# Kernel optimization log

Measured on AMD Instinct MI355X. Metric: run time of the kernel, lower is better.

The kernel has to match this reference:

```python
import jax, jax.numpy as jnp
import numpy as np
from jax import lax

L, B, T_IMG, T_TXT = 12, 2, 256, 64
E, H, G = 1024, 16, 2730
V = 16416  # image_vocab_count + 1
C = E // H
EPS = 1e-6  # flax LayerNorm default


def _ln(x, scale, bias):
    mu = jnp.mean(x, -1, keepdims=True)
    var = jnp.var(x, -1, keepdims=True)
    y = (x - mu) * lax.rsqrt(var + EPS)
    if scale is not None:
        y = y * scale
    if bias is not None:
        y = y + bias
    return y


def _attend(k, v, q, mask, o_w):
    # k,v: [B,K,H,C]  q: [B,Q,H,C]  mask: [B,K]
    bias = jnp.where(mask, 0.0, -jnp.inf)[:, None, None, :]
    w = jnp.einsum('bqhc,bkhc->bhqk', q, k) + bias
    w = jax.nn.softmax(w, axis=-1)
    out = jnp.einsum('bhqk,bkhc->bqhc', w, v)
    return out.reshape(out.shape[0], out.shape[1], E) @ o_w


def setup_inputs():
    key = jax.random.key(0)
    ks = jax.random.split(key, 16)
    s = 0.02
    n = lambda k, shape: jax.random.normal(k, shape, jnp.float32) * s
    return dict(
        encoder_state=n(ks[0], (B, T_TXT, E)),
        keys_state=jnp.zeros((L, B, T_IMG, H, C), jnp.float32),
        values_state=jnp.zeros((L, B, T_IMG, H, C), jnp.float32),
        attention_mask=jnp.ones((B, T_TXT), jnp.bool_),
        prev_token=5000,
        token_index=100,
        embed_tok=n(ks[1], (V, E)),
        embed_pos=n(ks[2], (T_IMG, E)),
        ln_emb_s=jnp.ones((E,), jnp.float32),
        ln_emb_b=jnp.zeros((E,), jnp.float32),
        final_ln_b=jnp.zeros((E,), jnp.float32),
        lm_head_w=n(ks[3], (E, V)),
        pre_sa_ln_b=jnp.zeros((L, E), jnp.float32),
        sa_q_w=n(ks[4], (L, E, E)), sa_k_w=n(ks[5], (L, E, E)),
        sa_v_w=n(ks[6], (L, E, E)), sa_o_w=n(ks[7], (L, E, E)),
        sa_ln_s=jnp.ones((L, E), jnp.float32), sa_ln_b=jnp.zeros((L, E), jnp.float32),
        pre_ca_ln_b=jnp.zeros((L, E), jnp.float32),
        ca_q_w=n(ks[8], (L, E, E)), ca_k_w=n(ks[9], (L, E, E)),
        ca_v_w=n(ks[10], (L, E, E)), ca_o_w=n(ks[11], (L, E, E)),
        ca_ln_s=jnp.ones((L, E), jnp.float32), ca_ln_b=jnp.zeros((L, E), jnp.float32),
        glu_ln0_b=jnp.zeros((L, E), jnp.float32),
        glu_fc0_w=n(ks[12], (L, E, G)), glu_fc1_w=n(ks[13], (L, E, G)),
        glu_ln1_b=jnp.zeros((L, G), jnp.float32),
        glu_fc2_w=n(ks[14], (L, G, E)),
    )


def _decode_step(encoder_state, keys_state, values_state, attention_mask,
                 prev_token, token_index, embed_tok, embed_pos,
                 ln_emb_s, ln_emb_b, final_ln_b, lm_head_w, layer_params):
    ones = jnp.ones((B, 1), jnp.int32)
    ds = embed_tok[prev_token * ones] + embed_pos[token_index * ones]  # [B,1,E]
    ds = _ln(ds, ln_emb_s, ln_emb_b)
    self_mask = jnp.broadcast_to(jnp.arange(T_IMG) < token_index + 1, (B, T_IMG))
    scale = C ** 0.5

    def step(ds, xs):
        ks_l, vs_l, p = xs  # per-layer KV cache [B,T_IMG,H,C] and params
        (pre_sa_b, qw, kw, vw, ow, sa_s, sa_b,
         pre_ca_b, cqw, ckw, cvw, cow, ca_s, ca_b,
         g0b, f0, f1, g1b, f2) = p
        # --- self attention with KV-cache append ---
        residual = ds
        x = _ln(ds, None, pre_sa_b)
        ks_l = lax.dynamic_update_slice(ks_l, (x @ kw).reshape(B, 1, H, C), (0, token_index, 0, 0))
        vs_l = lax.dynamic_update_slice(vs_l, (x @ vw).reshape(B, 1, H, C), (0, token_index, 0, 0))
        q = (x @ qw).reshape(B, 1, H, C) / scale
        x = _attend(ks_l, vs_l, q, self_mask, ow)
        ds = residual + _ln(x, sa_s, sa_b)
        # --- cross attention over encoder state ---
        residual = ds
        x = _ln(ds, None, pre_ca_b)
        ek = (encoder_state @ ckw).reshape(B, T_TXT, H, C)
        ev = (encoder_state @ cvw).reshape(B, T_TXT, H, C)
        q = (x @ cqw).reshape(B, 1, H, C) / scale
        x = _attend(ek, ev, q, attention_mask, cow)
        ds = residual + _ln(x, ca_s, ca_b)
        # --- GLU FFN ---
        residual = ds
        z = _ln(ds, None, g0b)
        w = jax.nn.gelu(z @ f0, approximate=False)
        z = _ln(w * (z @ f1), None, g1b)
        ds = residual + z @ f2
        return ds, (ks_l, vs_l)

    ds, (keys_state, values_state) = lax.scan(step, ds, (keys_state, values_state, layer_params))
    ds = _ln(ds, None, final_ln_b)
    logits = ds @ lm_head_w  # [B,1,V]
    return logits, keys_state, values_state


def reference(encoder_state, keys_state, values_state, attention_mask, prev_token,
              token_index, embed_tok, embed_pos, ln_emb_s, ln_emb_b, final_ln_b,
              lm_head_w, pre_sa_ln_b, sa_q_w, sa_k_w, sa_v_w, sa_o_w, sa_ln_s,
              sa_ln_b, pre_ca_ln_b, ca_q_w, ca_k_w, ca_v_w, ca_o_w, ca_ln_s,
              ca_ln_b, glu_ln0_b, glu_fc0_w, glu_fc1_w, glu_ln1_b, glu_fc2_w):
    layer_params = (pre_sa_ln_b, sa_q_w, sa_k_w, sa_v_w, sa_o_w, sa_ln_s, sa_ln_b,
                    pre_ca_ln_b, ca_q_w, ca_k_w, ca_v_w, ca_o_w, ca_ln_s, ca_ln_b,
                    glu_ln0_b, glu_fc0_w, glu_fc1_w, glu_ln1_b, glu_fc2_w)
    return _decode_step(encoder_state, keys_state, values_state, attention_mask,
                        prev_token, token_index, embed_tok, embed_pos,
                        ln_emb_s, ln_emb_b, final_ln_b, lm_head_w, layer_params)
```

## Files before the change

### kernel.cpp

```cpp
#include <hip/hip_runtime.h>
#include <math.h>

#define LAYERS 12
#define EE 1024
#define GG 2730
#define VV 16416
#define EPS 1e-6f

#define OFF_DS 0
#define NSLOT 37
#define OFF_ACC (OFF_DS + NSLOT*2048)
#define ACC_STRIDE 28672
#define AQ 0
#define AK 2048
#define AV 4096
#define AY 6144
#define ASC 10240
#define AOUT 12288
#define AY2 14336
#define AA 16384
#define AB2 21844
#define ACC_TOTAL (LAYERS*ACC_STRIDE)
#define ZERO_FLOATS (NSLOT*2048 + ACC_TOTAL)

#define KVL 524288
#define KVB 262144

struct MegaP {
  const float* enc; const float* keys_in; const float* values_in;
  const int* maski; const int* pt; const int* ti;
  const float* tok; const float* pos; const float* ln_s; const float* ln_b;
  const float* final_b; const float* lm_w;
  const float* pre_sa_b; const float* saq; const float* sak; const float* sav;
  const float* sao; const float* sas; const float* sab;
  const float* pre_ca_b; const float* caq; const float* ckw; const float* cvw;
  const float* cao; const float* cas; const float* cab;
  const float* g0b; const float* f0; const float* f1; const float* g1b; const float* f2;
  float* logits; float* keys_out; float* values_out; float* ws;
};

__device__ __forceinline__ void red4(float* sm, float& a, float& b, float& c, float& d){
  #pragma unroll
  for(int o=32;o;o>>=1){ a+=__shfl_down(a,o); b+=__shfl_down(b,o); c+=__shfl_down(c,o); d+=__shfl_down(d,o); }
  int w=threadIdx.x>>6, l=threadIdx.x&63;
  __syncthreads();
  if(l==0){ sm[w]=a; sm[4+w]=b; sm[8+w]=c; sm[12+w]=d; }
  __syncthreads();
  a=sm[0]+sm[1]+sm[2]+sm[3]; b=sm[4]+sm[5]+sm[6]+sm[7];
  c=sm[8]+sm[9]+sm[10]+sm[11]; d=sm[12]+sm[13]+sm[14]+sm[15];
}

__device__ __forceinline__ void ln_stats_g(const float* v, int K, float* sm,
    float& mu0, float& rs0, float& mu1, float& rs1){
  float s0=0,q0=0,s1=0,q1=0;
  for(int i=threadIdx.x;i<K;i+=256){ float a=v[i], b=v[K+i]; s0+=a;q0+=a*a;s1+=b;q1+=b*b; }
  red4(sm,s0,q0,s1,q1);
  mu0=s0/K; mu1=s1/K;
  rs0=rsqrtf(fmaxf(q0/K-mu0*mu0,0.f)+EPS);
  rs1=rsqrtf(fmaxf(q1/K-mu1*mu1,0.f)+EPS);
}

__device__ __forceinline__ void ln_stats_l(float (*Ds)[1024], float* sm,
    float& mu0, float& rs0, float& mu1, float& rs1){
  float s0=0,q0=0,s1=0,q1=0;
  for(int i=threadIdx.x;i<EE;i+=256){ float a=Ds[0][i], b=Ds[1][i]; s0+=a;q0+=a*a;s1+=b;q1+=b*b; }
  red4(sm,s0,q0,s1,q1);
  mu0=s0/EE; mu1=s1/EE;
  rs0=rsqrtf(fmaxf(q0/EE-mu0*mu0,0.f)+EPS);
  rs1=rsqrtf(fmaxf(q1/EE-mu1*mu1,0.f)+EPS);
}

__device__ __forceinline__ void build_ds3(const float* dsi, const float* accL,
    const float* sasl, const float* sabl, const float* casl, const float* cabl,
    float (*Ds)[1024], float* sm){
  float mu0,rs0,mu1,rs1;
  ln_stats_g(accL+AY, EE, sm, mu0,rs0,mu1,rs1);
  for(int i=threadIdx.x;i<EE;i+=256){ float sc=sasl[i], bi=sabl[i];
    Ds[0][i]=dsi[i]    + (accL[AY+i]-mu0)*rs0*sc + bi;
    Ds[1][i]=dsi[EE+i] + (accL[AY+EE+i]-mu1)*rs1*sc + bi; }
  ln_stats_g(accL+AY2, EE, sm, mu0,rs0,mu1,rs1);
  for(int i=threadIdx.x;i<EE;i+=256){ float sc=casl[i], bi=cabl[i];
    Ds[0][i] += (accL[AY2+i]-mu0)*rs0*sc + bi;
    Ds[1][i] += (accL[AY2+EE+i]-mu1)*rs1*sc + bi; }
}

__global__ __launch_bounds__(256)
void k_prelude(MegaP p){
  __shared__ float ev[EE];
  __shared__ float sm[16];
  const int t=threadIdx.x;
  int ptv = p.pt[0], tiv = p.ti[0];
  float s0=0,q0=0,d1=0,d2=0;
  for(int i=t;i<EE;i+=256){ float v=p.tok[(size_t)ptv*EE+i]+p.pos[(size_t)tiv*EE+i]; ev[i]=v; s0+=v; q0+=v*v; }
  red4(sm,s0,q0,d1,d2);
  float mu=s0/EE, rs=rsqrtf(fmaxf(q0/EE-mu*mu,0.f)+EPS);
  float* ds0 = p.ws + OFF_DS;
  __syncthreads();
  for(int i=t;i<EE;i+=256){ float y=(ev[i]-mu)*rs*p.ln_s[i]+p.ln_b[i]; ds0[i]=y; ds0[EE+i]=y; }
}

__global__ __launch_bounds__(256)
void k_qkv(MegaP p, int l){
  __shared__ float Xs[2][1024];
  __shared__ float sm[16];
  const int t=threadIdx.x, bx=blockIdx.x, by=blockIdx.y;
  if (bx >= 12){
    int cb = (bx-12)*64 + by;
    #pragma unroll
    for(int j=0;j<4;j++){
      int idx4 = cb*1024 + j*256 + t;
      int kv = idx4 >> 17;
      int r4 = idx4 & 131071;
      size_t off = (size_t)l*KVL + (size_t)r4*4;
      float4 v = *(const float4*)((kv? p.values_in : p.keys_in) + off);
      *(float4*)((kv? p.values_out : p.keys_out) + off) = v;
    }
    return;
  }
  const float* dsi = p.ws + OFF_DS + (size_t)(3*l)*2048;
  float* accL = p.ws + OFF_ACC + (size_t)l*ACC_STRIDE;
  const size_t lE2=(size_t)l*EE*EE, lE=(size_t)l*EE;
  int c = bx*256 + t;
  int sel = c>>10, cc = c&1023;
  const float* W = (sel==0? p.saq : sel==1? p.sak : p.sav) + lE2;
  float* O = accL + (sel==0? AQ : sel==1? AK : AV);
  int k0 = by*16;
  const float* wp = W + (size_t)k0*EE + cc;
  float wr[16];
  #pragma unroll
  for(int k=0;k<16;k++) wr[k] = wp[(size_t)k*EE];
  float mu0,rs0,mu1,rs1;
  ln_stats_g(dsi, EE, sm, mu0,rs0,mu1,rs1);
  for(int i=t;i<EE;i+=256){ float bi=p.pre_sa_b[lE+i];
    Xs[0][i]=(dsi[i]-mu0)*rs0+bi; Xs[1][i]=(dsi[EE+i]-mu1)*rs1+bi; }
  __syncthreads();
  float a0=0,a1=0;
  #pragma unroll
  for(int k=0;k<16;k++){ a0+=Xs[0][k0+k]*wr[k]; a1+=Xs[1][k0+k]*wr[k]; }
  atomicAdd(&O[cc],a0); atomicAdd(&O[EE+cc],a1);
}

__global__ __launch_bounds__(256)
void k_selfo(MegaP p, int l){
  __shared__ float Ds[2][1024];
  __shared__ float att[2][256];
  __shared__ float sm[16];
  const int t=threadIdx.x, bkid=blockIdx.x, tiv=p.ti[0];
  float* accL = p.ws + OFF_ACC + (size_t)l*ACC_STRIDE;
  const size_t lE2=(size_t)l*EE*EE;
  int cg=bkid&3, h=(bkid>>2)&15, sub=(bkid>>6)&3, hoff=h*64;
  if (t < 128){ int bb2=t>>6, c2=t&63; Ds[bb2][c2] = accL[AQ + bb2*EE + hoff + c2]*0.125f; }
  __syncthreads();
  for(int bb2=0;bb2<2;bb2++)
    for(int tt=t; tt<=tiv; tt+=256){
      const float* kr = (tt<tiv) ? (p.keys_in + (size_t)l*KVL + (size_t)bb2*KVB + (size_t)tt*EE + hoff)
                                 : (accL + AK + bb2*EE + hoff);
      float d=0;
      #pragma unroll
      for(int c2=0;c2<64;c2++) d += Ds[bb2][c2]*kr[c2];
      att[bb2][tt] = d;
    }
  __syncthreads();
  int wv=t>>6, l2=t&63;
  if (wv<2){
    float m=-3.4e38f;
    for(int tt=l2; tt<=tiv; tt+=64) m=fmaxf(m, att[wv][tt]);
    #pragma unroll
    for(int o=32;o;o>>=1) m=fmaxf(m,__shfl_xor(m,o));
    float s=0;
    for(int tt=l2; tt<=tiv; tt+=64){ float e=__expf(att[wv][tt]-m); att[wv][tt]=e; s+=e; }
    #pragma unroll
    for(int o=32;o;o>>=1) s+=__shfl_xor(s,o);
    if(l2==0) sm[8+wv]=1.f/s;
  }
  __syncthreads();
  {
    int bb2=t>>7, j=(t>>3)&15, part=t&7, colh=sub*16+j;
    float v=0;
    for(int tt=part; tt<=tiv; tt+=8){
      float vv = (tt<tiv)? p.values_in[(size_t)l*KVL + (size_t)bb2*KVB + (size_t)tt*EE + hoff + colh]
                         : accL[AV + bb2*EE + hoff + colh];
      v += att[bb2][tt]*vv;
    }
    v += __shfl_down(v,4,8); v += __shfl_down(v,2,8); v += __shfl_down(v,1,8);
    if(part==0) Ds[bb2][512+j] = v*sm[8+bb2];
  }
  __syncthreads();
  {
    int c = cg*256+t, kb = hoff + sub*16;
    const float* wp = p.sao + lE2 + (size_t)kb*EE + c;
    float a0=0,a1=0;
    #pragma unroll
    for(int j2=0;j2<16;j2++){ float w=wp[(size_t)j2*EE]; a0+=Ds[0][512+j2]*w; a1+=Ds[1][512+j2]*w; }
    atomicAdd(&accL[AY+c],a0); atomicAdd(&accL[AY+EE+c],a1);
  }
  if (cg==0 && sub==0){
    int bb2=t>>7, kv=(t>>6)&1, c2=t&63;
    float val = accL[(kv?AV:AK) + bb2*EE + hoff + c2];
    float* dst = (kv? p.values_out : p.keys_out)
               + (size_t)l*KVL + (size_t)bb2*KVB + (size_t)tiv*EE + hoff + c2;
    *dst = val;
  }
}

__global__ __launch_bounds__(256)
void k_qscore(MegaP p, int l){
  __shared__ float Xs[1024];
  __shared__ float P[16][64];
  __shared__ float qs[64];
  __shared__ float us[256];
  __shared__ float sm[16];
  const int t=threadIdx.x, bh=blockIdx.x, ec=blockIdx.y;
  const int b=bh>>4, h=bh&15, hoff=h*64;
  float* accL = p.ws + OFF_ACC + (size_t)l*ACC_STRIDE;
  const float* dsi = p.ws + OFF_DS + (size_t)(3*l)*2048;
  const size_t lE2=(size_t)l*EE*EE, lE=(size_t)l*EE;
  const int w=t>>6, ln=t&63;

  float s0=0,q0=0;
  for(int i=t;i<EE;i+=256){ float v=accL[AY+b*EE+i]; s0+=v; q0+=v*v; }
  #pragma unroll
  for(int o=32;o;o>>=1){ s0+=__shfl_down(s0,o); q0+=__shfl_down(q0,o); }
  if(ln==0){ sm[w]=s0; sm[4+w]=q0; }
  __syncthreads();
  float mu=(sm[0]+sm[1]+sm[2]+sm[3])/EE;
  float qq=(sm[4]+sm[5]+sm[6]+sm[7])/EE;
  float rs=rsqrtf(fmaxf(qq-mu*mu,0.f)+EPS);
  float s1=0,q1=0;
  for(int i=t;i<EE;i+=256){
    float d = dsi[b*EE+i] + (accL[AY+b*EE+i]-mu)*rs*p.sas[lE+i] + p.sab[lE+i];
    Xs[i]=d; s1+=d; q1+=d*d;
  }
  #pragma unroll
  for(int o=32;o;o>>=1){ s1+=__shfl_down(s1,o); q1+=__shfl_down(q1,o); }
  if(ln==0){ sm[8+w]=s1; sm[12+w]=q1; }
  __syncthreads();
  float mu2=(sm[8]+sm[9]+sm[10]+sm[11])/EE;
  float q2=(sm[12]+sm[13]+sm[14]+sm[15])/EE;
  float rs2=rsqrtf(fmaxf(q2-mu2*mu2,0.f)+EPS);
  for(int i=t;i<EE;i+=256) Xs[i] = (Xs[i]-mu2)*rs2 + p.pre_ca_b[lE+i];
  __syncthreads();

  {
    int c4=t&15, kr=t>>4;
    const float4* cq = (const float4*)(p.caq + lE2 + (size_t)kr*EE + hoff) + c4;
    float ax=0,ay=0,az=0,aw=0;
    #pragma unroll 8
    for(int i=0;i<64;i++){
      float4 wv = cq[(size_t)i*16*256];
      float x = Xs[kr+16*i];
      ax+=x*wv.x; ay+=x*wv.y; az+=x*wv.z; aw+=x*wv.w;
    }
    P[kr][c4*4+0]=ax; P[kr][c4*4+1]=ay; P[kr][c4*4+2]=az; P[kr][c4*4+3]=aw;
  }
  __syncthreads();
  if (t<64){
    float qv=0;
    #pragma unroll
    for(int kr=0;kr<16;kr++) qv += P[kr][t];
    qs[t] = qv*0.125f;
  }
  __syncthreads();

  {
    const float4* ckp = (const float4*)(p.ckw + lE2 + (size_t)(ec*256+t)*EE + hoff);
    float u=0;
    #pragma unroll
    for(int j=0;j<16;j++){
      float4 wv=ckp[j];
      u += wv.x*qs[4*j] + wv.y*qs[4*j+1] + wv.z*qs[4*j+2] + wv.w*qs[4*j+3];
    }
    us[t]=u;
  }
  __syncthreads();

  int t2=t&63, q4=t>>6;
  const float4* ep = (const float4*)(p.enc + (size_t)(b*64+t2)*EE + ec*256 + q4*64);
  float pa=0;
  #pragma unroll
  for(int j=0;j<16;j++){
    float4 e4=ep[j];
    pa += e4.x*us[q4*64+4*j] + e4.y*us[q4*64+4*j+1] + e4.z*us[q4*64+4*j+2] + e4.w*us[q4*64+4*j+3];
  }
  atomicAdd(&accL[ASC + (b*16+h)*64 + t2], pa);
}

__global__ __launch_bounds__(256)
void k_ov(MegaP p, int l){
  __shared__ float att[64];
  __shared__ float ctxp[2][128];
  __shared__ float ctxs[128];
  __shared__ float smr[2];
  const int t=threadIdx.x, bh=blockIdx.x, es=blockIdx.y;
  const int b=bh>>4, h=bh&15, hoff=h*64, e0=es*128;
  float* accL = p.ws + OFF_ACC + (size_t)l*ACC_STRIDE;
  const size_t lE2=(size_t)l*EE*EE;
  const int c=t&63, part=t>>6;
  const float* vp = p.cvw + lE2 + (size_t)(e0+part*32)*EE + hoff + c;
  float wr[32];
  #pragma unroll
  for(int j=0;j<32;j++) wr[j] = vp[(size_t)j*EE];
  if (t<64){
    float sc = accL[ASC + (b*16+h)*64 + t];
    int mi=b*64+t;
    bool valid = (p.maski[mi]!=0) || (((const unsigned char*)p.maski)[mi]!=0);
    sc = valid? sc : -3.4e38f;
    float m=sc;
    #pragma unroll
    for(int o=32;o;o>>=1) m=fmaxf(m,__shfl_xor(m,o));
    float e_ = valid? __expf(sc-m) : 0.f;
    float s=e_;
    #pragma unroll
    for(int o=32;o;o>>=1) s+=__shfl_xor(s,o);
    att[t]=e_;
    if(t==0) smr[0]=1.f/s;
  }
  __syncthreads();
  {
    int e2=t>>1, half=t&1;
    const float* ep = p.enc + (size_t)(b*64+half*32)*EE + e0+e2;
    float ca=0;
    #pragma unroll 8
    for(int tt=0;tt<32;tt++) ca += att[half*32+tt]*ep[(size_t)tt*EE];
    ctxp[half][e2]=ca;
  }
  __syncthreads();
  if (t<128) ctxs[t] = (ctxp[0][t]+ctxp[1][t])*smr[0];
  __syncthreads();
  float a=0;
  #pragma unroll
  for(int j=0;j<32;j++) a += ctxs[part*32+j]*wr[j];
  atomicAdd(&accL[AOUT + b*EE + hoff + c], a);
}

__global__ __launch_bounds__(256)
void k_y2(MegaP p, int l){
  __shared__ float Xs[2][1024];
  const int t=threadIdx.x;
  float* accL = p.ws + OFF_ACC + (size_t)l*ACC_STRIDE;
  const size_t lE2=(size_t)l*EE*EE;
  int c = blockIdx.x*256 + t;
  int k0 = blockIdx.y*16;
  const float* wp = p.cao + lE2 + (size_t)k0*EE + c;
  float wr[16];
  #pragma unroll
  for(int k=0;k<16;k++) wr[k] = wp[(size_t)k*EE];
  for(int i=t;i<EE;i+=256){ Xs[0][i]=accL[AOUT+i]; Xs[1][i]=accL[AOUT+EE+i]; }
  __syncthreads();
  float a0=0,a1=0;
  #pragma unroll
  for(int k=0;k<16;k++){ a0+=Xs[0][k0+k]*wr[k]; a1+=Xs[1][k0+k]*wr[k]; }
  atomicAdd(&accL[AY2+c],a0); atomicAdd(&accL[AY2+EE+c],a1);
}

__global__ __launch_bounds__(256)
void k_glu01(MegaP p, int l){
  __shared__ float Xs[2][1024];
  __shared__ float Ds[2][1024];
  __shared__ float sm[16];
  const int t=threadIdx.x;
  const float* dsi = p.ws + OFF_DS + (size_t)(3*l)*2048;
  float* accL = p.ws + OFF_ACC + (size_t)l*ACC_STRIDE;
  const size_t lEG=(size_t)l*EE*GG, lE=(size_t)l*EE;
  int c2 = blockIdx.x*256 + t;
  int k0 = blockIdx.y*16;
  int sel=0, col=0;
  const float* W = nullptr;
  float2 wr[16];
  if (c2 < 2730){
    sel = (c2>=1365); int cc2 = sel? c2-1365 : c2; col = cc2*2;
    W = (sel? p.f1 : p.f0) + lEG;
    const float2* wp = (const float2*)(W + (size_t)k0*GG + col);
    #pragma unroll
    for(int k=0;k<16;k++) wr[k] = wp[(size_t)k*1365];
  }
  build_ds3(dsi, accL, p.sas+lE, p.sab+lE, p.cas+lE, p.cab+lE, Ds, sm);
  float mu0,rs0,mu1,rs1;
  ln_stats_l(Ds, sm, mu0,rs0,mu1,rs1);
  for(int i=t;i<EE;i+=256){ float bi=p.g0b[lE+i];
    Xs[0][i]=(Ds[0][i]-mu0)*rs0+bi; Xs[1][i]=(Ds[1][i]-mu1)*rs1+bi; }
  __syncthreads();
  if (c2 < 2730){
    float* O = accL + (sel? AB2 : AA);
    float a0=0,a1=0,b0=0,b1=0;
    #pragma unroll
    for(int k=0;k<16;k++){
      float x0=Xs[0][k0+k], x1=Xs[1][k0+k];
      a0+=x0*wr[k].x; a1+=x0*wr[k].y; b0+=x1*wr[k].x; b1+=x1*wr[k].y;
    }
    atomicAdd(&O[col+0],a0); atomicAdd(&O[col+1],a1);
    atomicAdd(&O[GG+col+0],b0); atomicAdd(&O[GG+col+1],b1);
  }
}

__global__ __launch_bounds__(256)
void k_glu2(MegaP p, int l){
  __shared__ float Xs[2][2736];
  __shared__ float Ds[2][1024];
  __shared__ float sm[16];
  const int t=threadIdx.x;
  const float* dsi = p.ws + OFF_DS + (size_t)(3*l)*2048;
  float* ds4 = p.ws + OFF_DS + (size_t)(3*l+3)*2048;
  float* accL = p.ws + OFF_ACC + (size_t)l*ACC_STRIDE;
  const size_t lGE=(size_t)l*GG*EE, lE=(size_t)l*EE, lG=(size_t)l*GG;
  const int ks = blockIdx.y;
  int c = blockIdx.x*256 + t;
  int k0 = ks*32, k1 = k0+32; if (k1>GG) k1=GG;
  const float* wp = p.f2 + lGE + (size_t)k0*EE + c;
  float wr[32];
  #pragma unroll
  for(int k=0;k<32;k++) wr[k] = (k0+k<GG) ? wp[(size_t)k*EE] : 0.f;
  if (ks==0) build_ds3(dsi, accL, p.sas+lE, p.sab+lE, p.cas+lE, p.cab+lE, Ds, sm);
  float s0=0,q0=0,s1=0,q1=0;
  for(int i=t;i<GG;i+=256){
    float a0v=accL[AA+i], a1v=accL[AA+GG+i];
    float b0v=accL[AB2+i], b1v=accL[AB2+GG+i];
    float g0v=0.5f*a0v*(1.f+erff(a0v*0.70710678118654752f));
    float g1v=0.5f*a1v*(1.f+erff(a1v*0.70710678118654752f));
    float t0=g0v*b0v, t1=g1v*b1v;
    Xs[0][i]=t0; Xs[1][i]=t1;
    s0+=t0;q0+=t0*t0;s1+=t1;q1+=t1*t1;
  }
  red4(sm,s0,q0,s1,q1);
  float mu0=s0/GG, mu1=s1/GG;
  float rs0=rsqrtf(fmaxf(q0/GG-mu0*mu0,0.f)+EPS), rs1=rsqrtf(fmaxf(q1/GG-mu1*mu1,0.f)+EPS);
  for(int i=t;i<GG;i+=256){ float bi=p.g1b[lG+i];
    Xs[0][i]=(Xs[0][i]-mu0)*rs0+bi; Xs[1][i]=(Xs[1][i]-mu1)*rs1+bi; }
  __syncthreads();
  float a0=0,b0=0;
  if (ks==0){ a0=Ds[0][c]; b0=Ds[1][c]; }
  #pragma unroll
  for(int k=0;k<32;k++){
    if (k0+k<GG){ a0+=Xs[0][k0+k]*wr[k]; b0+=Xs[1][k0+k]*wr[k]; }
  }
  atomicAdd(&ds4[c],a0); atomicAdd(&ds4[EE+c],b0);
}

__global__ __launch_bounds__(256)
void k_lm(MegaP p){
  __shared__ float Xs[2][1024];
  __shared__ float sm[16];
  const int t=threadIdx.x;
  const float* dsf = p.ws + OFF_DS + (size_t)36*2048;
  float mu0,rs0,mu1,rs1;
  ln_stats_g(dsf, EE, sm, mu0,rs0,mu1,rs1);
  for(int i=t;i<EE;i+=256){ float bi=p.final_b[i];
    Xs[0][i]=(dsf[i]-mu0)*rs0+bi; Xs[1][i]=(dsf[EE+i]-mu1)*rs1+bi; }
  __syncthreads();
  int c4 = blockIdx.x*256 + t;
  if (c4 < 4104){
    int col = c4*4;
    int k0 = blockIdx.y*32;
    const float4* wp = (const float4*)(p.lm_w + (size_t)k0*VV + col);
    float a0=0,a1=0,a2=0,a3=0,b0=0,b1=0,b2=0,b3=0;
    #pragma unroll 8
    for(int k=0;k<32;k++){
      float4 w=*wp; wp+=4104;
      float x0=Xs[0][k0+k], x1=Xs[1][k0+k];
      a0+=x0*w.x; a1+=x0*w.y; a2+=x0*w.z; a3+=x0*w.w;
      b0+=x1*w.x; b1+=x1*w.y; b2+=x1*w.z; b3+=x1*w.w;
    }
    atomicAdd(&p.logits[col+0],a0); atomicAdd(&p.logits[col+1],a1);
    atomicAdd(&p.logits[col+2],a2); atomicAdd(&p.logits[col+3],a3);
    atomicAdd(&p.logits[VV+col+0],b0); atomicAdd(&p.logits[VV+col+1],b1);
    atomicAdd(&p.logits[VV+col+2],b2); atomicAdd(&p.logits[VV+col+3],b3);
  }
}

extern "C" void kernel_launch(void* const* d_in, const int* in_sizes, int n_in,
                              void* d_out, int out_size, void* d_ws, size_t ws_size,
                              hipStream_t stream){
  (void)in_sizes; (void)n_in; (void)out_size; (void)ws_size;
  float* out = (float*)d_out;
  float* ws = (float*)d_ws;

  MegaP P;
  P.enc        = (const float*)d_in[0];
  P.keys_in    = (const float*)d_in[1];
  P.values_in  = (const float*)d_in[2];
  P.maski      = (const int*)d_in[3];
  P.pt         = (const int*)d_in[4];
  P.ti         = (const int*)d_in[5];
  P.tok        = (const float*)d_in[6];
  P.pos        = (const float*)d_in[7];
  P.ln_s       = (const float*)d_in[8];
  P.ln_b       = (const float*)d_in[9];
  P.final_b    = (const float*)d_in[10];
  P.lm_w       = (const float*)d_in[11];
  P.pre_sa_b   = (const float*)d_in[12];
  P.saq        = (const float*)d_in[13];
  P.sak        = (const float*)d_in[14];
  P.sav        = (const float*)d_in[15];
  P.sao        = (const float*)d_in[16];
  P.sas        = (const float*)d_in[17];
  P.sab        = (const float*)d_in[18];
  P.pre_ca_b   = (const float*)d_in[19];
  P.caq        = (const float*)d_in[20];
  P.ckw        = (const float*)d_in[21];
  P.cvw        = (const float*)d_in[22];
  P.cao        = (const float*)d_in[23];
  P.cas        = (const float*)d_in[24];
  P.cab        = (const float*)d_in[25];
  P.g0b        = (const float*)d_in[26];
  P.f0         = (const float*)d_in[27];
  P.f1         = (const float*)d_in[28];
  P.g1b        = (const float*)d_in[29];
  P.f2         = (const float*)d_in[30];
  P.logits     = out;
  P.keys_out   = out + (size_t)2*VV;
  P.values_out = P.keys_out + (size_t)LAYERS*KVL;
  P.ws         = ws;

  hipMemsetAsync(ws + OFF_DS, 0, (size_t)ZERO_FLOATS*sizeof(float), stream);
  hipMemsetAsync(P.logits, 0, (size_t)2*VV*sizeof(float), stream);

  k_prelude<<<1,256,0,stream>>>(P);
  for (int l=0;l<LAYERS;l++){
    k_qkv   <<<dim3(16,64),256,0,stream>>>(P,l);
    k_selfo <<<256,        256,0,stream>>>(P,l);
    k_qscore<<<dim3(32,4), 256,0,stream>>>(P,l);
    k_ov    <<<dim3(32,8), 256,0,stream>>>(P,l);
    k_y2    <<<dim3(4,64), 256,0,stream>>>(P,l);
    k_glu01 <<<dim3(11,64),256,0,stream>>>(P,l);
    k_glu2  <<<dim3(4,86), 256,0,stream>>>(P,l);
  }
  k_lm<<<dim3(17,32),256,0,stream>>>(P);
}
```

Measured before the change: 1.075 ms.

## Fuse all per-layer kernels into one persistent megakernel with grid barriers

Replaces the 86 separate kernel launches (prelude, seven kernels per layer, LM head) with a single persistent kernel of 512 blocks that steps through the stages, separated by a two-level atomic grid barrier. The KV-cache copy moves into the prelude phase and is spread across all blocks. Work splits are retuned to fit the fixed block count. Cross-block data is read with relaxed atomic loads. The aim is to remove launch overhead and inter-kernel gaps. The risks are barrier cost, a deadlock hazard if the 512 blocks are not all co-resident (the spin has a timeout break that could silently corrupt results), and lower parallelism in some stages.

```diff
diff --git a/kernel.cpp b/kernel.cpp
--- a/kernel.cpp
+++ b/kernel.cpp
@@ -6,6 +6,9 @@
 #define GG 2730
 #define VV 16416
 #define EPS 1e-6f
+#define NBLK 512
+#define NGRP 32
+#define GRPSZ (NBLK/NGRP)
 
 #define OFF_DS 0
 #define NSLOT 37
@@ -21,7 +24,8 @@
 #define AA 16384
 #define AB2 21844
 #define ACC_TOTAL (LAYERS*ACC_STRIDE)
-#define ZERO_FLOATS (NSLOT*2048 + ACC_TOTAL)
+#define OFF_BAR (OFF_ACC + ACC_TOTAL)
+#define ZERO_FLOATS (NSLOT*2048 + ACC_TOTAL + 8192)
 
 #define KVL 524288
 #define KVB 262144
@@ -39,6 +43,34 @@
   float* logits; float* keys_out; float* values_out; float* ws;
 };
 
+__device__ __forceinline__ float gload(const float* p){
+  return __hip_atomic_load(p, __ATOMIC_RELAXED, __HIP_MEMORY_SCOPE_AGENT);
+}
+
+__device__ __forceinline__ void bar_sync(int* bar, int gen){
+  asm volatile("s_waitcnt vmcnt(0)" ::: "memory");
+  __syncthreads();
+  if (threadIdx.x==0){
+    int grp = blockIdx.x & (NGRP-1);
+    int v = __hip_atomic_fetch_add(&bar[grp*64], 1, __ATOMIC_RELAXED, __HIP_MEMORY_SCOPE_AGENT);
+    if (v == gen*GRPSZ + (GRPSZ-1)){
+      int m = __hip_atomic_fetch_add(&bar[2048], 1, __ATOMIC_RELAXED, __HIP_MEMORY_SCOPE_AGENT);
+      if (m == gen*NGRP + (NGRP-1)){
+        #pragma unroll 4
+        for (int q=0;q<NGRP;q++)
+          __hip_atomic_store(&bar[2112+q*64], gen+1, __ATOMIC_RELAXED, __HIP_MEMORY_SCOPE_AGENT);
+      }
+    }
+    int it=0;
+    while (__hip_atomic_load(&bar[2112+grp*64], __ATOMIC_RELAXED, __HIP_MEMORY_SCOPE_AGENT) <= gen){
+      __builtin_amdgcn_s_sleep(8);
+      if (++it > (1<<14)) break;
+    }
+  }
+  __syncthreads();
+  asm volatile("" ::: "memory");
+}
+
 __device__ __forceinline__ void red4(float* sm, float& a, float& b, float& c, float& d){
   #pragma unroll
   for(int o=32;o;o>>=1){ a+=__shfl_down(a,o); b+=__shfl_down(b,o); c+=__shfl_down(c,o); d+=__shfl_down(d,o); }
@@ -50,10 +82,10 @@
   c=sm[8]+sm[9]+sm[10]+sm[11]; d=sm[12]+sm[13]+sm[14]+sm[15];
 }
 
-__device__ __forceinline__ void ln_stats_g(const float* v, int K, float* sm,
+__device__ __forceinline__ void ln_stats_gl(const float* v, int K, float* sm,
     float& mu0, float& rs0, float& mu1, float& rs1){
   float s0=0,q0=0,s1=0,q1=0;
-  for(int i=threadIdx.x;i<K;i+=256){ float a=v[i], b=v[K+i]; s0+=a;q0+=a*a;s1+=b;q1+=b*b; }
+  for(int i=threadIdx.x;i<K;i+=256){ float a=gload(v+i), b=gload(v+K+i); s0+=a;q0+=a*a;s1+=b;q1+=b*b; }
   red4(sm,s0,q0,s1,q1);
   mu0=s0/K; mu1=s1/K;
   rs0=rsqrtf(fmaxf(q0/K-mu0*mu0,0.f)+EPS);
@@ -70,400 +102,386 @@
   rs1=rsqrtf(fmaxf(q1/EE-mu1*mu1,0.f)+EPS);
 }
 
-__device__ __forceinline__ void build_ds3(const float* dsi, const float* accL,
+__device__ __forceinline__ void build_ds3_gl(const float* dsi, const float* accL,
     const float* sasl, const float* sabl, const float* casl, const float* cabl,
     float (*Ds)[1024], float* sm){
   float mu0,rs0,mu1,rs1;
-  ln_stats_g(accL+AY, EE, sm, mu0,rs0,mu1,rs1);
+  ln_stats_gl(accL+AY, EE, sm, mu0,rs0,mu1,rs1);
   for(int i=threadIdx.x;i<EE;i+=256){ float sc=sasl[i], bi=sabl[i];
-    Ds[0][i]=dsi[i]    + (accL[AY+i]-mu0)*rs0*sc + bi;
-    Ds[1][i]=dsi[EE+i] + (accL[AY+EE+i]-mu1)*rs1*sc + bi; }
-  ln_stats_g(accL+AY2, EE, sm, mu0,rs0,mu1,rs1);
+    Ds[0][i]=gload(dsi+i)    + (gload(accL+AY+i)-mu0)*rs0*sc + bi;
+    Ds[1][i]=gload(dsi+EE+i) + (gload(accL+AY+EE+i)-mu1)*rs1*sc + bi; }
+  ln_stats_gl(accL+AY2, EE, sm, mu0,rs0,mu1,rs1);
   for(int i=threadIdx.x;i<EE;i+=256){ float sc=casl[i], bi=cabl[i];
-    Ds[0][i] += (accL[AY2+i]-mu0)*rs0*sc + bi;
-    Ds[1][i] += (accL[AY2+EE+i]-mu1)*rs1*sc + bi; }
-}
-
-__global__ __launch_bounds__(256)
-void k_prelude(MegaP p){
-  __shared__ float ev[EE];
-  __shared__ float sm[16];
-  const int t=threadIdx.x;
-  int ptv = p.pt[0], tiv = p.ti[0];
-  float s0=0,q0=0,d1=0,d2=0;
-  for(int i=t;i<EE;i+=256){ float v=p.tok[(size_t)ptv*EE+i]+p.pos[(size_t)tiv*EE+i]; ev[i]=v; s0+=v; q0+=v*v; }
-  red4(sm,s0,q0,d1,d2);
-  float mu=s0/EE, rs=rsqrtf(fmaxf(q0/EE-mu*mu,0.f)+EPS);
-  float* ds0 = p.ws + OFF_DS;
-  __syncthreads();
-  for(int i=t;i<EE;i+=256){ float y=(ev[i]-mu)*rs*p.ln_s[i]+p.ln_b[i]; ds0[i]=y; ds0[EE+i]=y; }
-}
-
-__global__ __launch_bounds__(256)
-void k_qkv(MegaP p, int l){
-  __shared__ float Xs[2][1024];
-  __shared__ float sm[16];
-  const int t=threadIdx.x, bx=blockIdx.x, by=blockIdx.y;
-  if (bx >= 12){
-    int cb = (bx-12)*64 + by;
-    #pragma unroll
-    for(int j=0;j<4;j++){
-      int idx4 = cb*1024 + j*256 + t;
-      int kv = idx4 >> 17;
-      int r4 = idx4 & 131071;
-      size_t off = (size_t)l*KVL + (size_t)r4*4;
-      float4 v = *(const float4*)((kv? p.values_in : p.keys_in) + off);
-      *(float4*)((kv? p.values_out : p.keys_out) + off) = v;
-    }
-    return;
+    Ds[0][i] += (gload(accL+AY2+i)-mu0)*rs0*sc + bi;
+    Ds[1][i] += (gload(accL+AY2+EE+i)-mu1)*rs1*sc + bi; }
+}
+
+__global__ __launch_bounds__(256, 2)
+void k_mega(MegaP p){
+  __shared__ float LB[7536];
+  const int t = threadIdx.x;
+  const int bkid = blockIdx.x;
+  int* bar = (int*)(p.ws + OFF_BAR);
+  const int tiv = p.ti[0];
+  int g = 0;
+
+  if (bkid==0){
+    float* ev = LB; float* sm = LB+1024;
+    int ptv = p.pt[0];
+    float s0=0,q0=0,d1=0,d2=0;
+    for(int i=t;i<EE;i+=256){ float v=p.tok[(size_t)ptv*EE+i]+p.pos[(size_t)tiv*EE+i]; ev[i]=v; s0+=v; q0+=v*v; }
+    red4(sm,s0,q0,d1,d2);
+    float mu=s0/EE, rs=rsqrtf(fmaxf(q0/EE-mu*mu,0.f)+EPS);
+    float* ds0 = p.ws + OFF_DS;
+    __syncthreads();
+    for(int i=t;i<EE;i+=256){ float y=(ev[i]-mu)*rs*p.ln_s[i]+p.ln_b[i]; atomicAdd(&ds0[i],y); atomicAdd(&ds0[EE+i],y); }
+  } else {
+    for (int i=(bkid-1)*256+t; i<3145728; i+=511*256){
+      int kv = (i>=1572864);
+      int r = i - (kv?1572864:0);
+      int ll=r>>17, r2=r&131071, bb=r2>>16, r3=r2&65535, tt=r3>>8, e4=r3&255;
+      if (tt==tiv) continue;
+      size_t off=(size_t)ll*KVL+(size_t)bb*KVB+(size_t)tt*EE+(size_t)e4*4;
+      float4 v=*(const float4*)((kv?p.values_in:p.keys_in)+off);
+      *(float4*)((kv?p.values_out:p.keys_out)+off)=v;
+    }
   }
-  const float* dsi = p.ws + OFF_DS + (size_t)(3*l)*2048;
-  float* accL = p.ws + OFF_ACC + (size_t)l*ACC_STRIDE;
-  const size_t lE2=(size_t)l*EE*EE, lE=(size_t)l*EE;
-  int c = bx*256 + t;
-  int sel = c>>10, cc = c&1023;
-  const float* W = (sel==0? p.saq : sel==1? p.sak : p.sav) + lE2;
-  float* O = accL + (sel==0? AQ : sel==1? AK : AV);
-  int k0 = by*16;
-  const float* wp = W + (size_t)k0*EE + cc;
-  float wr[16];
-  #pragma unroll
-  for(int k=0;k<16;k++) wr[k] = wp[(size_t)k*EE];
-  float mu0,rs0,mu1,rs1;
-  ln_stats_g(dsi, EE, sm, mu0,rs0,mu1,rs1);
-  for(int i=t;i<EE;i+=256){ float bi=p.pre_sa_b[lE+i];
-    Xs[0][i]=(dsi[i]-mu0)*rs0+bi; Xs[1][i]=(dsi[EE+i]-mu1)*rs1+bi; }
-  __syncthreads();
-  float a0=0,a1=0;
-  #pragma unroll
-  for(int k=0;k<16;k++){ a0+=Xs[0][k0+k]*wr[k]; a1+=Xs[1][k0+k]*wr[k]; }
-  atomicAdd(&O[cc],a0); atomicAdd(&O[EE+cc],a1);
-}
-
-__global__ __launch_bounds__(256)
-void k_selfo(MegaP p, int l){
-  __shared__ float Ds[2][1024];
-  __shared__ float att[2][256];
-  __shared__ float sm[16];
-  const int t=threadIdx.x, bkid=blockIdx.x, tiv=p.ti[0];
-  float* accL = p.ws + OFF_ACC + (size_t)l*ACC_STRIDE;
-  const size_t lE2=(size_t)l*EE*EE;
-  int cg=bkid&3, h=(bkid>>2)&15, sub=(bkid>>6)&3, hoff=h*64;
-  if (t < 128){ int bb2=t>>6, c2=t&63; Ds[bb2][c2] = accL[AQ + bb2*EE + hoff + c2]*0.125f; }
-  __syncthreads();
-  for(int bb2=0;bb2<2;bb2++)
-    for(int tt=t; tt<=tiv; tt+=256){
-      const float* kr = (tt<tiv) ? (p.keys_in + (size_t)l*KVL + (size_t)bb2*KVB + (size_t)tt*EE + hoff)
-                                 : (accL + AK + bb2*EE + hoff);
-      float d=0;
-      #pragma unroll
-      for(int c2=0;c2<64;c2++) d += Ds[bb2][c2]*kr[c2];
-      att[bb2][tt] = d;
-    }
-  __syncthreads();
-  int wv=t>>6, l2=t&63;
-  if (wv<2){
-    float m=-3.4e38f;
-    for(int tt=l2; tt<=tiv; tt+=64) m=fmaxf(m, att[wv][tt]);
-    #pragma unroll
-    for(int o=32;o;o>>=1) m=fmaxf(m,__shfl_xor(m,o));
-    float s=0;
-    for(int tt=l2; tt<=tiv; tt+=64){ float e=__expf(att[wv][tt]-m); att[wv][tt]=e; s+=e; }
-    #pragma unroll
-    for(int o=32;o;o>>=1) s+=__shfl_xor(s,o);
-    if(l2==0) sm[8+wv]=1.f/s;
+  bar_sync(bar, g++);
+
+  for (int l=0;l<LAYERS;l++){
+    float* accL = p.ws + OFF_ACC + (size_t)l*ACC_STRIDE;
+    const float* dsi = p.ws + OFF_DS + (size_t)(3*l)*2048;
+    float* ds4 = p.ws + OFF_DS + (size_t)(3*l+3)*2048;
+    const size_t lE2=(size_t)l*EE*EE, lE=(size_t)l*EE;
+    const size_t lEG=(size_t)l*EE*GG, lGE=(size_t)l*GG*EE, lG=(size_t)l*GG;
+
+    if (bkid < 492){
+      float* Xs0=LB; float* Xs1=LB+1024; float* sm=LB+2048;
+      int cg=bkid%12, ks=bkid/12;
+      int c=cg*256+t, sel=c>>10, cc=c&1023;
+      const float* W = (sel==0? p.saq : sel==1? p.sak : p.sav) + lE2;
+      float* O = accL + (sel==0? AQ : sel==1? AK : AV);
+      int k0=ks*25;
+      const float* wp = W + (size_t)k0*EE + cc;
+      float wr[25];
+      #pragma unroll
+      for(int k=0;k<25;k++) wr[k] = (k0+k<EE)? wp[(size_t)k*EE] : 0.f;
+      float mu0,rs0,mu1,rs1;
+      ln_stats_gl(dsi, EE, sm, mu0,rs0,mu1,rs1);
+      for(int i=t;i<EE;i+=256){ float bi=p.pre_sa_b[lE+i];
+        Xs0[i]=(gload(dsi+i)-mu0)*rs0+bi; Xs1[i]=(gload(dsi+EE+i)-mu1)*rs1+bi; }
+      __syncthreads();
+      float a0=0,a1=0;
+      #pragma unroll
+      for(int k=0;k<25;k++){ if(k0+k<EE){ a0+=Xs0[k0+k]*wr[k]; a1+=Xs1[k0+k]*wr[k]; } }
+      atomicAdd(&O[cc],a0); atomicAdd(&O[EE+cc],a1);
+    }
+    bar_sync(bar, g++);
+
+    if (bkid < 256){
+      float (*Ds)[1024] = (float(*)[1024])LB;
+      float (*att)[256] = (float(*)[256])(LB+2048);
+      float* sm = LB+2560;
+      int cg=bkid&3, h=(bkid>>2)&15, sub=(bkid>>6)&3, hoff=h*64;
+      if (t < 128){ int bb2=t>>6, c2=t&63; Ds[bb2][c2] = gload(accL+AQ+bb2*EE+hoff+c2)*0.125f; }
+      __syncthreads();
+      for(int bb2=0;bb2<2;bb2++)
+        for(int tt=t; tt<=tiv; tt+=256){
+          float d=0;
+          if (tt<tiv){
+            const float* kr = p.keys_in + (size_t)l*KVL + (size_t)bb2*KVB + (size_t)tt*EE + hoff;
+            #pragma unroll
+            for(int c2=0;c2<64;c2++) d += Ds[bb2][c2]*kr[c2];
+          } else {
+            const float* kr = accL + AK + bb2*EE + hoff;
+            #pragma unroll
+            for(int c2=0;c2<64;c2++) d += Ds[bb2][c2]*gload(kr+c2);
+          }
+          att[bb2][tt] = d;
+        }
+      __syncthreads();
+      int wv=t>>6, l2=t&63;
+      if (wv<2){
+        float m=-3.4e38f;
+        for(int tt=l2; tt<=tiv; tt+=64) m=fmaxf(m, att[wv][tt]);
+        #pragma unroll
+        for(int o=32;o;o>>=1) m=fmaxf(m,__shfl_xor(m,o));
+        float s=0;
+        for(int tt=l2; tt<=tiv; tt+=64){ float e=__expf(att[wv][tt]-m); att[wv][tt]=e; s+=e; }
+        #pragma unroll
+        for(int o=32;o;o>>=1) s+=__shfl_xor(s,o);
+        if(l2==0) sm[8+wv]=1.f/s;
+      }
+      __syncthreads();
+      {
+        int bb2=t>>7, j=(t>>3)&15, part=t&7, colh=sub*16+j;
+        float v=0;
+        for(int tt=part; tt<=tiv; tt+=8){
+          float vv = (tt<tiv)? p.values_in[(size_t)l*KVL + (size_t)bb2*KVB + (size_t)tt*EE + hoff + colh]
+                             : gload(accL+AV+bb2*EE+hoff+colh);
+          v += att[bb2][tt]*vv;
+        }
+        v += __shfl_down(v,4,8); v += __shfl_down(v,2,8); v += __shfl_down(v,1,8);
+        if(part==0) Ds[bb2][512+j] = v*sm[8+bb2];
+      }
+      __syncthreads();
+      {
+        int c = cg*256+t, kb = hoff + sub*16;
+        const float* wp = p.sao + lE2 + (size_t)kb*EE + c;
+        float a0=0,a1=0;
+        #pragma unroll
+        for(int j2=0;j2<16;j2++){ float w=wp[(size_t)j2*EE]; a0+=Ds[0][512+j2]*w; a1+=Ds[1][512+j2]*w; }
+        atomicAdd(&accL[AY+c],a0); atomicAdd(&accL[AY+EE+c],a1);
+      }
+      if (cg==0 && sub==0){
+        int bb2=t>>7, kv=(t>>6)&1, c2=t&63;
+        float val = gload(accL + (kv?AV:AK) + bb2*EE + hoff + c2);
+        float* dst = (kv? p.values_out : p.keys_out)
+                   + (size_t)l*KVL + (size_t)bb2*KVB + (size_t)tiv*EE + hoff + c2;
+        *dst = val;
+      }
+    }
+    bar_sync(bar, g++);
+
+    if (bkid < 128){
+      float* Xs = LB; float* Pq = LB+1024; float* qs = LB+2048;
+      float* us = LB+2112; float* sm = LB+2368;
+      int bh=bkid>>2, ec=bkid&3;
+      int b=bh>>4, h=bh&15, hoff=h*64;
+      const int w=t>>6, ln=t&63;
+      float s0=0,q0=0;
+      for(int i=t;i<EE;i+=256){ float v=gload(accL+AY+b*EE+i); s0+=v; q0+=v*v; }
+      #pragma unroll
+      for(int o=32;o;o>>=1){ s0+=__shfl_down(s0,o); q0+=__shfl_down(q0,o); }
+      if(ln==0){ sm[w]=s0; sm[4+w]=q0; }
+      __syncthreads();
+      float mu=(sm[0]+sm[1]+sm[2]+sm[3])/EE;
+      float qq=(sm[4]+sm[5]+sm[6]+sm[7])/EE;
+      float rs=rsqrtf(fmaxf(qq-mu*mu,0.f)+EPS);
+      float s1=0,q1=0;
+      for(int i=t;i<EE;i+=256){
+        float d = gload(dsi+b*EE+i) + (gload(accL+AY+b*EE+i)-mu)*rs*p.sas[lE+i] + p.sab[lE+i];
+        Xs[i]=d; s1+=d; q1+=d*d;
+      }
+      #pragma unroll
+      for(int o=32;o;o>>=1){ s1+=__shfl_down(s1,o); q1+=__shfl_down(q1,o); }
+      if(ln==0){ sm[8+w]=s1; sm[12+w]=q1; }
+      __syncthreads();
+      float mu2=(sm[8]+sm[9]+sm[10]+sm[11])/EE;
+      float q2=(sm[12]+sm[13]+sm[14]+sm[15])/EE;
+      float rs2=rsqrtf(fmaxf(q2-mu2*mu2,0.f)+EPS);
+      for(int i=t;i<EE;i+=256) Xs[i] = (Xs[i]-mu2)*rs2 + p.pre_ca_b[lE+i];
+      __syncthreads();
+      {
+        int c4=t&15, kr=t>>4;
+        const float4* cq = (const float4*)(p.caq + lE2 + (size_t)kr*EE + hoff) + c4;
+        float ax=0,ay=0,az=0,aw=0;
+        #pragma unroll 8
+        for(int i=0;i<64;i++){
+          float4 wv = cq[(size_t)i*16*256];
+          float x = Xs[kr+16*i];
+          ax+=x*wv.x; ay+=x*wv.y; az+=x*wv.z; aw+=x*wv.w;
+        }
+        Pq[kr*64+c4*4+0]=ax; Pq[kr*64+c4*4+1]=ay; Pq[kr*64+c4*4+2]=az; Pq[kr*64+c4*4+3]=aw;
+      }
+      __syncthreads();
+      if (t<64){
+        float qv=0;
+        #pragma unroll
+        for(int kr=0;kr<16;kr++) qv += Pq[kr*64+t];
+        qs[t] = qv*0.125f;
+      }
+      __syncthreads();
+      {
+        const float4* ckp = (const float4*)(p.ckw + lE2 + (size_t)(ec*256+t)*EE + hoff);
+        float u=0;
+        #pragma unroll
+        for(int j=0;j<16;j++){
+          float4 wv=ckp[j];
+          u += wv.x*qs[4*j] + wv.y*qs[4*j+1] + wv.z*qs[4*j+2] + wv.w*qs[4*j+3];
+        }
+        us[t]=u;
+      }
+      __syncthreads();
+      int t2=t&63, q4=t>>6;
+      const float4* ep = (const float4*)(p.enc + (size_t)(b*64+t2)*EE + ec*256 + q4*64);
+      float pa=0;
+      #pragma unroll
+      for(int j=0;j<16;j++){
+        float4 e4=ep[j];
+        pa += e4.x*us[q4*64+4*j] + e4.y*us[q4*64+4*j+1] + e4.z*us[q4*64+4*j+2] + e4.w*us[q4*64+4*j+3];
+      }
+      atomicAdd(&accL[ASC + (b*16+h)*64 + t2], pa);
+    }
+    bar_sync(bar, g++);
+
+    if (bkid < 256){
+      float* att = LB; float* ctxp = LB+64; float* ctxs = LB+320; float* smr = LB+448;
+      int bh=bkid>>3, es=bkid&7;
+      int b=bh>>4, h=bh&15, hoff=h*64, e0=es*128;
+      const int c=t&63, part=t>>6;
+      const float* vp = p.cvw + lE2 + (size_t)(e0+part*32)*EE + hoff + c;
+      float wr[32];
+      #pragma unroll
+      for(int j=0;j<32;j++) wr[j] = vp[(size_t)j*EE];
+      if (t<64){
+        float sc = gload(accL + ASC + (b*16+h)*64 + t);
+        int mi=b*64+t;
+        bool valid = (p.maski[mi]!=0) || (((const unsigned char*)p.maski)[mi]!=0);
+        sc = valid? sc : -3.4e38f;
+        float m=sc;
+        #pragma unroll
+        for(int o=32;o;o>>=1) m=fmaxf(m,__shfl_xor(m,o));
+        float e_ = valid? __expf(sc-m) : 0.f;
+        float s=e_;
+        #pragma unroll
+        for(int o=32;o;o>>=1) s+=__shfl_xor(s,o);
+        att[t]=e_;
+        if(t==0) smr[0]=1.f/s;
+      }
+      __syncthreads();
+      {
+        int e2=t>>1, half=t&1;
+        const float* ep = p.enc + (size_t)(b*64+half*32)*EE + e0+e2;
+        float ca=0;
+        #pragma unroll 8
+        for(int tt=0;tt<32;tt++) ca += att[half*32+tt]*ep[(size_t)tt*EE];
+        ctxp[half*128+e2]=ca;
+      }
+      __syncthreads();
+      if (t<128) ctxs[t] = (ctxp[t]+ctxp[128+t])*smr[0];
+      __syncthreads();
+      float a=0;
+      #pragma unroll
+      for(int j=0;j<32;j++) a += ctxs[part*32+j]*wr[j];
+      atomicAdd(&accL[AOUT + b*EE + hoff + c], a);
+    }
+    bar_sync(bar, g++);
+
+    if (bkid < 256){
+      float* Xs0=LB; float* Xs1=LB+1024;
+      int cg=bkid&3, ks=bkid>>2;
+      int c = cg*256 + t;
+      int k0 = ks*16;
+      const float* wp = p.cao + lE2 + (size_t)k0*EE + c;
+      float wr[16];
+      #pragma unroll
+      for(int k=0;k<16;k++) wr[k] = wp[(size_t)k*EE];
+      for(int i=t;i<EE;i+=256){ Xs0[i]=gload(accL+AOUT+i); Xs1[i]=gload(accL+AOUT+EE+i); }
+      __syncthreads();
+      float a0=0,a1=0;
+      #pragma unroll
+      for(int k=0;k<16;k++){ a0+=Xs0[k0+k]*wr[k]; a1+=Xs1[k0+k]*wr[k]; }
+      atomicAdd(&accL[AY2+c],a0); atomicAdd(&accL[AY2+EE+c],a1);
+    }
+    bar_sync(bar, g++);
+
+    if (bkid < 495){
+      float* Xs0=LB; float* Xs1=LB+1024;
+      float (*Ds)[1024]=(float(*)[1024])(LB+2048);
+      float* sm=LB+4096;
+      int cg=bkid%11, ks=bkid/11;
+      int c2 = cg*256 + t;
+      int k0 = ks*23;
+      int sel=0, col=0;
+      float2 wr[23];
+      if (c2 < 2730){
+        sel = (c2>=1365); int cc2 = sel? c2-1365 : c2; col = cc2*2;
+        const float* W = (sel? p.f1 : p.f0) + lEG;
+        const float2* wp = (const float2*)(W + (size_t)k0*GG + col);
+        #pragma unroll
+        for(int k=0;k<23;k++) wr[k] = (k0+k<EE)? wp[(size_t)k*1365] : make_float2(0.f,0.f);
+      }
+      build_ds3_gl(dsi, accL, p.sas+lE, p.sab+lE, p.cas+lE, p.cab+lE, Ds, sm);
+      float mu0,rs0,mu1,rs1;
+      ln_stats_l(Ds, sm, mu0,rs0,mu1,rs1);
+      for(int i=t;i<EE;i+=256){ float bi=p.g0b[lE+i];
+        Xs0[i]=(Ds[0][i]-mu0)*rs0+bi; Xs1[i]=(Ds[1][i]-mu1)*rs1+bi; }
+      __syncthreads();
+      if (c2 < 2730){
+        float* O = accL + (sel? AB2 : AA);
+        float a0=0,a1=0,b0=0,b1=0;
+        #pragma unroll
+        for(int k=0;k<23;k++){
+          if (k0+k<EE){
+            float x0=Xs0[k0+k], x1=Xs1[k0+k];
+            a0+=x0*wr[k].x; a1+=x0*wr[k].y; b0+=x1*wr[k].x; b1+=x1*wr[k].y;
+          }
+        }
+        atomicAdd(&O[col+0],a0); atomicAdd(&O[col+1],a1);
+        atomicAdd(&O[GG+col+0],b0); atomicAdd(&O[GG+col+1],b1);
+      }
+    }
+    bar_sync(bar, g++);
+
+    if (bkid < 256){
+      float* Xs0=LB; float* Xs1=LB+2736;
+      float (*Ds)[1024]=(float(*)[1024])(LB+5472);
+      float* sm=LB+7520;
+      int cg=bkid&3, ks=bkid>>2;
+      int c = cg*256 + t;
+      int k0 = ks*43;
+      const float* wp = p.f2 + lGE + (size_t)k0*EE + c;
+      float wr[43];
+      #pragma unroll
+      for(int k=0;k<43;k++) wr[k] = (k0+k<GG)? wp[(size_t)k*EE] : 0.f;
+      if (ks==0) build_ds3_gl(dsi, accL, p.sas+lE, p.sab+lE, p.cas+lE, p.cab+lE, Ds, sm);
+      float s0=0,q0=0,s1=0,q1=0;
+      for(int i=t;i<GG;i+=256){
+        float a0v=gload(accL+AA+i), a1v=gload(accL+AA+GG+i);
+        float b0v=gload(accL+AB2+i), b1v=gload(accL+AB2+GG+i);
+        float g0v=0.5f*a0v*(1.f+erff(a0v*0.70710678118654752f));
+        float g1v=0.5f*a1v*(1.f+erff(a1v*0.70710678118654752f));
+        float t0=g0v*b0v, t1=g1v*b1v;
+        Xs0[i]=t0; Xs1[i]=t1;
+        s0+=t0;q0+=t0*t0;s1+=t1;q1+=t1*t1;
+      }
+      red4(sm,s0,q0,s1,q1);
+      float mu0=s0/GG, mu1=s1/GG;
+      float rs0=rsqrtf(fmaxf(q0/GG-mu0*mu0,0.f)+EPS), rs1=rsqrtf(fmaxf(q1/GG-mu1*mu1,0.f)+EPS);
+      for(int i=t;i<GG;i+=256){ float bi=p.g1b[lG+i];
+        Xs0[i]=(Xs0[i]-mu0)*rs0+bi; Xs1[i]=(Xs1[i]-mu1)*rs1+bi; }
+      __syncthreads();
+      float a0=0,b0=0;
+      if (ks==0){ a0=Ds[0][c]; b0=Ds[1][c]; }
+      #pragma unroll
+      for(int k=0;k<43;k++){
+        if (k0+k<GG){ a0+=Xs0[k0+k]*wr[k]; b0+=Xs1[k0+k]*wr[k]; }
+      }
+      atomicAdd(&ds4[c],a0); atomicAdd(&ds4[EE+c],b0);
+    }
+    bar_sync(bar, g++);
   }
-  __syncthreads();
-  {
-    int bb2=t>>7, j=(t>>3)&15, part=t&7, colh=sub*16+j;
-    float v=0;
-    for(int tt=part; tt<=tiv; tt+=8){
-      float vv = (tt<tiv)? p.values_in[(size_t)l*KVL + (size_t)bb2*KVB + (size_t)tt*EE + hoff + colh]
-                         : accL[AV + bb2*EE + hoff + colh];
-      v += att[bb2][tt]*vv;
-    }
-    v += __shfl_down(v,4,8); v += __shfl_down(v,2,8); v += __shfl_down(v,1,8);
-    if(part==0) Ds[bb2][512+j] = v*sm[8+bb2];
-  }
-  __syncthreads();
-  {
-    int c = cg*256+t, kb = hoff + sub*16;
-    const float* wp = p.sao + lE2 + (size_t)kb*EE + c;
-    float a0=0,a1=0;
-    #pragma unroll
-    for(int j2=0;j2<16;j2++){ float w=wp[(size_t)j2*EE]; a0+=Ds[0][512+j2]*w; a1+=Ds[1][512+j2]*w; }
-    atomicAdd(&accL[AY+c],a0); atomicAdd(&accL[AY+EE+c],a1);
-  }
-  if (cg==0 && sub==0){
-    int bb2=t>>7, kv=(t>>6)&1, c2=t&63;
-    float val = accL[(kv?AV:AK) + bb2*EE + hoff + c2];
-    float* dst = (kv? p.values_out : p.keys_out)
-               + (size_t)l*KVL + (size_t)bb2*KVB + (size_t)tiv*EE + hoff + c2;
-    *dst = val;
-  }
-}
-
-__global__ __launch_bounds__(256)
-void k_qscore(MegaP p, int l){
-  __shared__ float Xs[1024];
-  __shared__ float P[16][64];
-  __shared__ float qs[64];
-  __shared__ float us[256];
-  __shared__ float sm[16];
-  const int t=threadIdx.x, bh=blockIdx.x, ec=blockIdx.y;
-  const int b=bh>>4, h=bh&15, hoff=h*64;
-  float* accL = p.ws + OFF_ACC + (size_t)l*ACC_STRIDE;
-  const float* dsi = p.ws + OFF_DS + (size_t)(3*l)*2048;
-  const size_t lE2=(size_t)l*EE*EE, lE=(size_t)l*EE;
-  const int w=t>>6, ln=t&63;
-
-  float s0=0,q0=0;
-  for(int i=t;i<EE;i+=256){ float v=accL[AY+b*EE+i]; s0+=v; q0+=v*v; }
-  #pragma unroll
-  for(int o=32;o;o>>=1){ s0+=__shfl_down(s0,o); q0+=__shfl_down(q0,o); }
-  if(ln==0){ sm[w]=s0; sm[4+w]=q0; }
-  __syncthreads();
-  float mu=(sm[0]+sm[1]+sm[2]+sm[3])/EE;
-  float qq=(sm[4]+sm[5]+sm[6]+sm[7])/EE;
-  float rs=rsqrtf(fmaxf(qq-mu*mu,0.f)+EPS);
-  float s1=0,q1=0;
-  for(int i=t;i<EE;i+=256){
-    float d = dsi[b*EE+i] + (accL[AY+b*EE+i]-mu)*rs*p.sas[lE+i] + p.sab[lE+i];
-    Xs[i]=d; s1+=d; q1+=d*d;
-  }
-  #pragma unroll
-  for(int o=32;o;o>>=1){ s1+=__shfl_down(s1,o); q1+=__shfl_down(q1,o); }
-  if(ln==0){ sm[8+w]=s1; sm[12+w]=q1; }
-  __syncthreads();
-  float mu2=(sm[8]+sm[9]+sm[10]+sm[11])/EE;
-  float q2=(sm[12]+sm[13]+sm[14]+sm[15])/EE;
-  float rs2=rsqrtf(fmaxf(q2-mu2*mu2,0.f)+EPS);
-  for(int i=t;i<EE;i+=256) Xs[i] = (Xs[i]-mu2)*rs2 + p.pre_ca_b[lE+i];
-  __syncthreads();
-
-  {
-    int c4=t&15, kr=t>>4;
-    const float4* cq = (const float4*)(p.caq + lE2 + (size_t)kr*EE + hoff) + c4;
-    float ax=0,ay=0,az=0,aw=0;
-    #pragma unroll 8
-    for(int i=0;i<64;i++){
-      float4 wv = cq[(size_t)i*16*256];
-      float x = Xs[kr+16*i];
-      ax+=x*wv.x; ay+=x*wv.y; az+=x*wv.z; aw+=x*wv.w;
-    }
-    P[kr][c4*4+0]=ax; P[kr][c4*4+1]=ay; P[kr][c4*4+2]=az; P[kr][c4*4+3]=aw;
-  }
-  __syncthreads();
-  if (t<64){
-    float qv=0;
-    #pragma unroll
-    for(int kr=0;kr<16;kr++) qv += P[kr][t];
-    qs[t] = qv*0.125f;
-  }
-  __syncthreads();
-
-  {
-    const float4* ckp = (const float4*)(p.ckw + lE2 + (size_t)(ec*256+t)*EE + hoff);
-    float u=0;
-    #pragma unroll
-    for(int j=0;j<16;j++){
-      float4 wv=ckp[j];
-      u += wv.x*qs[4*j] + wv.y*qs[4*j+1] + wv.z*qs[4*j+2] + wv.w*qs[4*j+3];
-    }
-    us[t]=u;
-  }
-  __syncthreads();
-
-  int t2=t&63, q4=t>>6;
-  const float4* ep = (const float4*)(p.enc + (size_t)(b*64+t2)*EE + ec*256 + q4*64);
-  float pa=0;
-  #pragma unroll
-  for(int j=0;j<16;j++){
-    float4 e4=ep[j];
-    pa += e4.x*us[q4*64+4*j] + e4.y*us[q4*64+4*j+1] + e4.z*us[q4*64+4*j+2] + e4.w*us[q4*64+4*j+3];
-  }
-  atomicAdd(&accL[ASC + (b*16+h)*64 + t2], pa);
-}
-
-__global__ __launch_bounds__(256)
-void k_ov(MegaP p, int l){
-  __shared__ float att[64];
-  __shared__ float ctxp[2][128];
-  __shared__ float ctxs[128];
-  __shared__ float smr[2];
-  const int t=threadIdx.x, bh=blockIdx.x, es=blockIdx.y;
-  const int b=bh>>4, h=bh&15, hoff=h*64, e0=es*128;
-  float* accL = p.ws + OFF_ACC + (size_t)l*ACC_STRIDE;
-  const size_t lE2=(size_t)l*EE*EE;
-  const int c=t&63, part=t>>6;
-  const float* vp = p.cvw + lE2 + (size_t)(e0+part*32)*EE + hoff + c;
-  float wr[32];
-  #pragma unroll
-  for(int j=0;j<32;j++) wr[j] = vp[(size_t)j*EE];
-  if (t<64){
-    float sc = accL[ASC + (b*16+h)*64 + t];
-    int mi=b*64+t;
-    bool valid = (p.maski[mi]!=0) || (((const unsigned char*)p.maski)[mi]!=0);
-    sc = valid? sc : -3.4e38f;
-    float m=sc;
-    #pragma unroll
-    for(int o=32;o;o>>=1) m=fmaxf(m,__shfl_xor(m,o));
-    float e_ = valid? __expf(sc-m) : 0.f;
-    float s=e_;
-    #pragma unroll
-    for(int o=32;o;o>>=1) s+=__shfl_xor(s,o);
-    att[t]=e_;
-    if(t==0) smr[0]=1.f/s;
-  }
-  __syncthreads();
-  {
-    int e2=t>>1, half=t&1;
-    const float* ep = p.enc + (size_t)(b*64+half*32)*EE + e0+e2;
-    float ca=0;
-    #pragma unroll 8
-    for(int tt=0;tt<32;tt++) ca += att[half*32+tt]*ep[(size_t)tt*EE];
-    ctxp[half][e2]=ca;
-  }
-  __syncthreads();
-  if (t<128) ctxs[t] = (ctxp[0][t]+ctxp[1][t])*smr[0];
-  __syncthreads();
-  float a=0;
-  #pragma unroll
-  for(int j=0;j<32;j++) a += ctxs[part*32+j]*wr[j];
-  atomicAdd(&accL[AOUT + b*EE + hoff + c], a);
-}
-
-__global__ __launch_bounds__(256)
-void k_y2(MegaP p, int l){
-  __shared__ float Xs[2][1024];
-  const int t=threadIdx.x;
-  float* accL = p.ws + OFF_ACC + (size_t)l*ACC_STRIDE;
-  const size_t lE2=(size_t)l*EE*EE;
-  int c = blockIdx.x*256 + t;
-  int k0 = blockIdx.y*16;
-  const float* wp = p.cao + lE2 + (size_t)k0*EE + c;
-  float wr[16];
-  #pragma unroll
-  for(int k=0;k<16;k++) wr[k] = wp[(size_t)k*EE];
-  for(int i=t;i<EE;i+=256){ Xs[0][i]=accL[AOUT+i]; Xs[1][i]=accL[AOUT+EE+i]; }
-  __syncthreads();
-  float a0=0,a1=0;
-  #pragma unroll
-  for(int k=0;k<16;k++){ a0+=Xs[0][k0+k]*wr[k]; a1+=Xs[1][k0+k]*wr[k]; }
-  atomicAdd(&accL[AY2+c],a0); atomicAdd(&accL[AY2+EE+c],a1);
-}
-
-__global__ __launch_bounds__(256)
-void k_glu01(MegaP p, int l){
-  __shared__ float Xs[2][1024];
-  __shared__ float Ds[2][1024];
-  __shared__ float sm[16];
-  const int t=threadIdx.x;
-  const float* dsi = p.ws + OFF_DS + (size_t)(3*l)*2048;
-  float* accL = p.ws + OFF_ACC + (size_t)l*ACC_STRIDE;
-  const size_t lEG=(size_t)l*EE*GG, lE=(size_t)l*EE;
-  int c2 = blockIdx.x*256 + t;
-  int k0 = blockIdx.y*16;
-  int sel=0, col=0;
-  const float* W = nullptr;
-  float2 wr[16];
-  if (c2 < 2730){
-    sel = (c2>=1365); int cc2 = sel? c2-1365 : c2; col = cc2*2;
-    W = (sel? p.f1 : p.f0) + lEG;
-    const float2* wp = (const float2*)(W + (size_t)k0*GG + col);
-    #pragma unroll
-    for(int k=0;k<16;k++) wr[k] = wp[(size_t)k*1365];
-  }
-  build_ds3(dsi, accL, p.sas+lE, p.sab+lE, p.cas+lE, p.cab+lE, Ds, sm);
-  float mu0,rs0,mu1,rs1;
-  ln_stats_l(Ds, sm, mu0,rs0,mu1,rs1);
-  for(int i=t;i<EE;i+=256){ float bi=p.g0b[lE+i];
-    Xs[0][i]=(Ds[0][i]-mu0)*rs0+bi; Xs[1][i]=(Ds[1][i]-mu1)*rs1+bi; }
-  __syncthreads();
-  if (c2 < 2730){
-    float* O = accL + (sel? AB2 : AA);
-    float a0=0,a1=0,b0=0,b1=0;
-    #pragma unroll
-    for(int k=0;k<16;k++){
-      float x0=Xs[0][k0+k], x1=Xs[1][k0+k];
-      a0+=x0*wr[k].x; a1+=x0*wr[k].y; b0+=x1*wr[k].x; b1+=x1*wr[k].y;
-    }
-    atomicAdd(&O[col+0],a0); atomicAdd(&O[col+1],a1);
-    atomicAdd(&O[GG+col+0],b0); atomicAdd(&O[GG+col+1],b1);
-  }
-}
-
-__global__ __launch_bounds__(256)
-void k_glu2(MegaP p, int l){
-  __shared__ float Xs[2][2736];
-  __shared__ float Ds[2][1024];
-  __shared__ float sm[16];
-  const int t=threadIdx.x;
-  const float* dsi = p.ws + OFF_DS + (size_t)(3*l)*2048;
-  float* ds4 = p.ws + OFF_DS + (size_t)(3*l+3)*2048;
-  float* accL = p.ws + OFF_ACC + (size_t)l*ACC_STRIDE;
-  const size_t lGE=(size_t)l*GG*EE, lE=(size_t)l*EE, lG=(size_t)l*GG;
-  const int ks = blockIdx.y;
-  int c = blockIdx.x*256 + t;
-  int k0 = ks*32, k1 = k0+32; if (k1>GG) k1=GG;
-  const float* wp = p.f2 + lGE + (size_t)k0*EE + c;
-  float wr[32];
-  #pragma unroll
-  for(int k=0;k<32;k++) wr[k] = (k0+k<GG) ? wp[(size_t)k*EE] : 0.f;
-  if (ks==0) build_ds3(dsi, accL, p.sas+lE, p.sab+lE, p.cas+lE, p.cab+lE, Ds, sm);
-  float s0=0,q0=0,s1=0,q1=0;
-  for(int i=t;i<GG;i+=256){
-    float a0v=accL[AA+i], a1v=accL[AA+GG+i];
-    float b0v=accL[AB2+i], b1v=accL[AB2+GG+i];
-    float g0v=0.5f*a0v*(1.f+erff(a0v*0.70710678118654752f));
-    float g1v=0.5f*a1v*(1.f+erff(a1v*0.70710678118654752f));
-    float t0=g0v*b0v, t1=g1v*b1v;
-    Xs[0][i]=t0; Xs[1][i]=t1;
-    s0+=t0;q0+=t0*t0;s1+=t1;q1+=t1*t1;
-  }
-  red4(sm,s0,q0,s1,q1);
-  float mu0=s0/GG, mu1=s1/GG;
-  float rs0=rsqrtf(fmaxf(q0/GG-mu0*mu0,0.f)+EPS), rs1=rsqrtf(fmaxf(q1/GG-mu1*mu1,0.f)+EPS);
-  for(int i=t;i<GG;i+=256){ float bi=p.g1b[lG+i];
-    Xs[0][i]=(Xs[0][i]-mu0)*rs0+bi; Xs[1][i]=(Xs[1][i]-mu1)*rs1+bi; }
-  __syncthreads();
-  float a0=0,b0=0;
-  if (ks==0){ a0=Ds[0][c]; b0=Ds[1][c]; }
-  #pragma unroll
-  for(int k=0;k<32;k++){
-    if (k0+k<GG){ a0+=Xs[0][k0+k]*wr[k]; b0+=Xs[1][k0+k]*wr[k]; }
-  }
-  atomicAdd(&ds4[c],a0); atomicAdd(&ds4[EE+c],b0);
-}
-
-__global__ __launch_bounds__(256)
-void k_lm(MegaP p){
-  __shared__ float Xs[2][1024];
-  __shared__ float sm[16];
-  const int t=threadIdx.x;
-  const float* dsf = p.ws + OFF_DS + (size_t)36*2048;
-  float mu0,rs0,mu1,rs1;
-  ln_stats_g(dsf, EE, sm, mu0,rs0,mu1,rs1);
-  for(int i=t;i<EE;i+=256){ float bi=p.final_b[i];
-    Xs[0][i]=(dsf[i]-mu0)*rs0+bi; Xs[1][i]=(dsf[EE+i]-mu1)*rs1+bi; }
-  __syncthreads();
-  int c4 = blockIdx.x*256 + t;
-  if (c4 < 4104){
-    int col = c4*4;
-    int k0 = blockIdx.y*32;
-    const float4* wp = (const float4*)(p.lm_w + (size_t)k0*VV + col);
-    float a0=0,a1=0,a2=0,a3=0,b0=0,b1=0,b2=0,b3=0;
-    #pragma unroll 8
-    for(int k=0;k<32;k++){
-      float4 w=*wp; wp+=4104;
-      float x0=Xs[0][k0+k], x1=Xs[1][k0+k];
-      a0+=x0*w.x; a1+=x0*w.y; a2+=x0*w.z; a3+=x0*w.w;
-      b0+=x1*w.x; b1+=x1*w.y; b2+=x1*w.z; b3+=x1*w.w;
-    }
-    atomicAdd(&p.logits[col+0],a0); atomicAdd(&p.logits[col+1],a1);
-    atomicAdd(&p.logits[col+2],a2); atomicAdd(&p.logits[col+3],a3);
-    atomicAdd(&p.logits[VV+col+0],b0); atomicAdd(&p.logits[VV+col+1],b1);
-    atomicAdd(&p.logits[VV+col+2],b2); atomicAdd(&p.logits[VV+col+3],b3);
+
+  if (bkid < 510){
+    float* Xs0=LB; float* Xs1=LB+1024; float* sm=LB+2048;
+    const float* dsf = p.ws + OFF_DS + (size_t)36*2048;
+    int cg=bkid%17, ks=bkid/17;
+    int c4 = cg*256 + t;
+    int k0 = ks*35;
+    float mu0,rs0,mu1,rs1;
+    ln_stats_gl(dsf, EE, sm, mu0,rs0,mu1,rs1);
+    for(int i=t;i<EE;i+=256){ float bi=p.final_b[i];
+      Xs0[i]=(gload(dsf+i)-mu0)*rs0+bi; Xs1[i]=(gload(dsf+EE+i)-mu1)*rs1+bi; }
+    __syncthreads();
+    if (c4 < 4104){
+      int col = c4*4;
+      const float4* wp = (const float4*)(p.lm_w + (size_t)k0*VV + col);
+      float a0=0,a1=0,a2=0,a3=0,b0=0,b1=0,b2=0,b3=0;
+      #pragma unroll 5
+      for(int k=0;k<35;k++){
+        if (k0+k<EE){
+          float4 w=wp[(size_t)k*4104];
+          float x0=Xs0[k0+k], x1=Xs1[k0+k];
+          a0+=x0*w.x; a1+=x0*w.y; a2+=x0*w.z; a3+=x0*w.w;
+          b0+=x1*w.x; b1+=x1*w.y; b2+=x1*w.z; b3+=x1*w.w;
+        }
+      }
+      atomicAdd(&p.logits[col+0],a0); atomicAdd(&p.logits[col+1],a1);
+      atomicAdd(&p.logits[col+2],a2); atomicAdd(&p.logits[col+3],a3);
+      atomicAdd(&p.logits[VV+col+0],b0); atomicAdd(&p.logits[VV+col+1],b1);
+      atomicAdd(&p.logits[VV+col+2],b2); atomicAdd(&p.logits[VV+col+3],b3);
+    }
   }
 }
 
@@ -514,15 +532,5 @@
   hipMemsetAsync(ws + OFF_DS, 0, (size_t)ZERO_FLOATS*sizeof(float), stream);
   hipMemsetAsync(P.logits, 0, (size_t)2*VV*sizeof(float), stream);
 
-  k_prelude<<<1,256,0,stream>>>(P);
-  for (int l=0;l<LAYERS;l++){
-    k_qkv   <<<dim3(16,64),256,0,stream>>>(P,l);
-    k_selfo <<<256,        256,0,stream>>>(P,l);
-    k_qscore<<<dim3(32,4), 256,0,stream>>>(P,l);
-    k_ov    <<<dim3(32,8), 256,0,stream>>>(P,l);
-    k_y2    <<<dim3(4,64), 256,0,stream>>>(P,l);
-    k_glu01 <<<dim3(11,64),256,0,stream>>>(P,l);
-    k_glu2  <<<dim3(4,86), 256,0,stream>>>(P,l);
-  }
-  k_lm<<<dim3(17,32),256,0,stream>>>(P);
-}
+  k_mega<<<NBLK,256,0,stream>>>(P);
+}
```

Measured after the change: 1.630 ms. 51.7% more time.
